# Optimization experiments

Measured on AMD Instinct MI355X. Metric: run time of the kernel, lower is better.

## Reference

```python
import jax, jax.numpy as jnp
import numpy as np

B, S, D = 2, 4096, 768
H, DH = 12, 64
W = 256          # one-sided window (attention_window=512 // 2)
G = 8            # number of global tokens (first G positions)
NEG = -1e9


def setup_inputs() -> dict:
    key = jax.random.key(0)
    ks = jax.random.split(key, 8)
    hidden_states = jax.random.normal(ks[0], (B, S, D), dtype=jnp.float32)
    attention_mask = jnp.ones((B, S), dtype=jnp.float32)
    sc = 0.02
    Wq = jax.random.normal(ks[1], (D, D), dtype=jnp.float32) * sc
    Wk = jax.random.normal(ks[2], (D, D), dtype=jnp.float32) * sc
    Wv = jax.random.normal(ks[3], (D, D), dtype=jnp.float32) * sc
    Wqg = jax.random.normal(ks[4], (D, D), dtype=jnp.float32) * sc
    Wkg = jax.random.normal(ks[5], (D, D), dtype=jnp.float32) * sc
    Wvg = jax.random.normal(ks[6], (D, D), dtype=jnp.float32) * sc
    return {"hidden_states": hidden_states, "attention_mask": attention_mask,
            "Wq": Wq, "Wk": Wk, "Wv": Wv, "Wqg": Wqg, "Wkg": Wkg, "Wvg": Wvg}


def _heads(x):  # [B,S,D] -> [B,H,S,DH]
    return x.reshape(B, S, H, DH).transpose(0, 2, 1, 3)


def longformer_attn(hidden_states, attention_mask, Wq, Wk, Wv, Wqg, Wkg, Wvg):
    scale = 1.0 / jnp.sqrt(jnp.float32(DH))
    q = _heads(hidden_states @ Wq) * scale   # [B,H,S,DH]
    k = _heads(hidden_states @ Wk)
    v = _heads(hidden_states @ Wv)

    n = S // W                                # number of query chunks
    kp = jnp.pad(k, ((0, 0), (0, 0), (W, W), (0, 0)))
    vp = jnp.pad(v, ((0, 0), (0, 0), (W, W), (0, 0)))
    # window indices into padded seq: chunk i covers keys [i*W - W, i*W + 2W)
    idx = jnp.arange(n)[:, None] * W + jnp.arange(3 * W)[None, :]   # [n,3W]
    k_win = kp[:, :, idx]                     # [B,H,n,3W,DH]
    v_win = vp[:, :, idx]
    qc = q.reshape(B, H, n, W, DH)

    scores = jnp.einsum('bhnqd,bhnkd->bhnqk', qc, k_win)  # [B,H,n,W,3W]

    # masks: band (|key-query|<=W), valid key position, not a global key,
    # and key attention_mask
    rel = jnp.arange(3 * W)[None, :] - jnp.arange(W)[:, None]   # [W,3W] = k - q
    band = (rel >= 0) & (rel <= 2 * W)
    key_pos = idx - W                                           # [n,3W] real positions
    valid = (key_pos >= 0) & (key_pos < S) & (key_pos >= G)
    struct_mask = band[None, :, :] & valid[:, None, :]          # [n,W,3W]
    amp = jnp.pad(attention_mask, ((0, 0), (W, W)))
    am_win = amp[:, idx] > 0.5                                  # [B,n,3W]
    full_mask = struct_mask[None] & am_win[:, :, None, :]       # [B,n,W,3W]
    scores = jnp.where(full_mask[:, None], scores, NEG)

    # every query also attends to the G global keys (regular key projection)
    gk = k[:, :, :G]                                            # [B,H,G,DH]
    gscore = jnp.einsum('bhsd,bhgd->bhsg', q, gk).reshape(B, H, n, W, G)
    all_scores = jnp.concatenate([gscore, scores], axis=-1)     # [B,H,n,W,G+3W]
    probs = jax.nn.softmax(all_scores, axis=-1)

    gv = v[:, :, :G]
    out = (jnp.einsum('bhnqk,bhnkd->bhnqd', probs[..., G:], v_win)
           + jnp.einsum('bhnqg,bhgd->bhnqd', probs[..., :G], gv))
    out = out.reshape(B, H, S, DH)

    # global queries attend to ALL tokens with the *_global projections
    qg = _heads(hidden_states @ Wqg)[:, :, :G] * scale          # [B,H,G,DH]
    kg = _heads(hidden_states @ Wkg)
    vg = _heads(hidden_states @ Wvg)
    gs = jnp.einsum('bhgd,bhsd->bhgs', qg, kg)                  # [B,H,G,S]
    gs = jnp.where(attention_mask[:, None, None, :] > 0.5, gs, NEG)
    gp = jax.nn.softmax(gs, axis=-1)
    gout = jnp.einsum('bhgs,bhsd->bhgd', gp, vg)
    out = out.at[:, :, :G].set(gout)

    return out.transpose(0, 2, 1, 3).reshape(B, S, D)


def reference(hidden_states, attention_mask, Wq, Wk, Wv, Wqg, Wkg, Wvg):
    return longformer_attn(hidden_states, attention_mask, Wq, Wk, Wv, Wqg, Wkg, Wvg)
```

## Files before the change

### kernel.cpp

```cpp
#include <hip/hip_runtime.h>

#define B_ 2
#define S_ 4096
#define D_ 768
#define H_ 12
#define DH_ 64
#define W_ 256
#define G_ 8
#define NEG_ (-1e9f)
#define NC_ 64
#define CK_ 64
#define WQB 128
#define NT_ 11
#define NWIN (B_ * H_ * (S_ / WQB))

typedef __attribute__((ext_vector_type(4))) float f32x4;
typedef __attribute__((ext_vector_type(16))) float f32x16;
typedef __attribute__((ext_vector_type(8))) short s16x8;
typedef __attribute__((ext_vector_type(4))) short s16x4;
typedef unsigned short ushort_t;

__device__ __forceinline__ unsigned short f2bf(float f) {
    union { float f; unsigned u; } v; v.f = f;
    unsigned r = v.u + 0x7FFFu + ((v.u >> 16) & 1u);
    return (unsigned short)(r >> 16);
}
__device__ __forceinline__ float bf2f(unsigned short b) {
    union { unsigned u; float f; } v; v.u = ((unsigned)b) << 16;
    return v.f;
}
__device__ __forceinline__ float bfbits(unsigned u) {
    union { unsigned u; float f; } v; v.u = u;
    return v.f;
}
__device__ __forceinline__ unsigned cvtpk_bf16(float lo, float hi) {
    unsigned r;
    asm("v_cvt_pk_bf16_f32 %0, %1, %2" : "=v"(r) : "v"(lo), "v"(hi));
    return r;
}
__device__ __forceinline__ void gload16(const ushort_t* g, ushort_t* l) {
    __builtin_amdgcn_global_load_lds(
        (const __attribute__((address_space(1))) unsigned*)g,
        (__attribute__((address_space(3))) unsigned*)l, 16, 0, 0);
}
__device__ __forceinline__ float vmax16f(f32x16 v) {
    float a0 = fmaxf(v[0], v[1]), a1 = fmaxf(v[2], v[3]);
    float a2 = fmaxf(v[4], v[5]), a3 = fmaxf(v[6], v[7]);
    float a4 = fmaxf(v[8], v[9]), a5 = fmaxf(v[10], v[11]);
    float a6 = fmaxf(v[12], v[13]), a7 = fmaxf(v[14], v[15]);
    return fmaxf(fmaxf(fmaxf(a0, a1), fmaxf(a2, a3)),
                 fmaxf(fmaxf(a4, a5), fmaxf(a6, a7)));
}
__device__ __forceinline__ float vsum16f(f32x16 v) {
    float a0 = v[0] + v[1], a1 = v[2] + v[3];
    float a2 = v[4] + v[5], a3 = v[6] + v[7];
    float a4 = v[8] + v[9], a5 = v[10] + v[11];
    float a6 = v[12] + v[13], a7 = v[14] + v[15];
    return ((a0 + a1) + (a2 + a3)) + ((a4 + a5) + (a6 + a7));
}

__global__ __launch_bounds__(256) void fused_pre(const float* __restrict__ hs,
                                                 const float* __restrict__ W0,
                                                 const float* __restrict__ W1,
                                                 const float* __restrict__ W2,
                                                 const float* __restrict__ W3,
                                                 const float* __restrict__ W4,
                                                 const float* __restrict__ Wqg,
                                                 ushort_t* __restrict__ hs_bf,
                                                 ushort_t* __restrict__ wt,
                                                 float* __restrict__ qg) {
    __shared__ float smf[2 * D_];
    const int bid = blockIdx.x;
    const int t = threadIdx.x;

    if (bid < 3072) {
        const int i = bid * 256 + t;
        float4 a = *(const float4*)&hs[(size_t)i * 8];
        float4 c = *(const float4*)&hs[(size_t)i * 8 + 4];
        s16x8 o;
        o[0] = (short)f2bf(a.x); o[1] = (short)f2bf(a.y);
        o[2] = (short)f2bf(a.z); o[3] = (short)f2bf(a.w);
        o[4] = (short)f2bf(c.x); o[5] = (short)f2bf(c.y);
        o[6] = (short)f2bf(c.z); o[7] = (short)f2bf(c.w);
        *(s16x8*)&hs_bf[(size_t)i * 8] = o;
    } else if (bid < 5952) {
        const int bid2 = bid - 3072;
        const int w = bid2 / 576;
        const int rem = bid2 - w * 576;
        const int k0 = (rem / 24) * 32;
        const int n0 = (rem % 24) * 32;
        const float* Wsrc = (w == 0) ? W0 : (w == 1) ? W1 : (w == 2) ? W2 : (w == 3) ? W3 : W4;
        const float scl = (w == 0) ? 0.125f * 1.44269504f : 1.0f;
        const int r = t >> 3, c4 = (t & 7) * 4;
        float4 src = *(const float4*)&Wsrc[(size_t)(k0 + r) * D_ + n0 + c4];
        smf[r * 33 + c4 + 0] = src.x; smf[r * 33 + c4 + 1] = src.y;
        smf[r * 33 + c4 + 2] = src.z; smf[r * 33 + c4 + 3] = src.w;
        __syncthreads();
        s16x4 o;
        o[0] = (short)f2bf(smf[(c4 + 0) * 33 + r] * scl);
        o[1] = (short)f2bf(smf[(c4 + 1) * 33 + r] * scl);
        o[2] = (short)f2bf(smf[(c4 + 2) * 33 + r] * scl);
        o[3] = (short)f2bf(smf[(c4 + 3) * 33 + r] * scl);
        *(s16x4*)&wt[((size_t)(w * D_ + n0 + r)) * D_ + k0 + c4] = o;
    } else {
        const int bid3 = bid - 5952;
        const int rp = bid3 / 6;
        const int c0 = (bid3 - rp * 6) * 128;
        const int r = t >> 7, cl = t & 127;
        for (int i = t; i < 2 * D_; i += 256) {
            const int rr = i / D_, kk = i - rr * D_;
            const int row = rp * 2 + rr;
            const int b = row >> 3, g = row & 7;
            smf[rr * D_ + kk] = hs[((size_t)b * S_ + g) * D_ + kk];
        }
        __syncthreads();
        float a0 = 0.f, a1 = 0.f, a2 = 0.f, a3 = 0.f;
        const float* wp = &Wqg[c0 + cl];
        for (int kk = 0; kk < D_; kk += 4) {
            a0 += smf[r * D_ + kk + 0] * wp[(size_t)(kk + 0) * D_];
            a1 += smf[r * D_ + kk + 1] * wp[(size_t)(kk + 1) * D_];
            a2 += smf[r * D_ + kk + 2] * wp[(size_t)(kk + 2) * D_];
            a3 += smf[r * D_ + kk + 3] * wp[(size_t)(kk + 3) * D_];
        }
        const int row = rp * 2 + r;
        qg[(size_t)row * D_ + c0 + cl] = (a0 + a1 + a2 + a3) * 0.125f;
    }
}

__global__ __launch_bounds__(256, 2) void proj_mfma(const ushort_t* __restrict__ A,
                                                    const ushort_t* __restrict__ Bt,
                                                    ushort_t* __restrict__ oq,
                                                    ushort_t* __restrict__ ok,
                                                    ushort_t* __restrict__ ov,
                                                    ushort_t* __restrict__ okg,
                                                    ushort_t* __restrict__ ovg) {
    __shared__ char smem[34048];
    ushort_t* Al = (ushort_t*)smem;
    ushort_t* Bl = Al + 128 * 64;

    const int t = threadIdx.x;
    const int m0 = blockIdx.x * 128;
    const int n0 = blockIdx.y * 128;
    const int lane = t & 63;
    const int w = t >> 6;
    const int wm = (w >> 1) * 64, wn = (w & 1) * 64;
    const int ln = lane & 15, hi = lane >> 4;

    const int srow_in_call = lane >> 3;
    const int scol = ((lane & 7) ^ srow_in_call) * 8;

    f32x4 acc[4][4];
#pragma unroll
    for (int mi = 0; mi < 4; ++mi)
#pragma unroll
        for (int ni = 0; ni < 4; ++ni) acc[mi][ni] = (f32x4){0.f, 0.f, 0.f, 0.f};

    for (int k0 = 0; k0 < D_; k0 += 64) {
        __syncthreads();
#pragma unroll
        for (int j = 0; j < 4; ++j) {
            const int rbase = (w * 4 + j) * 8;
            const int row = rbase + srow_in_call;
            gload16(&A[(size_t)(m0 + row) * D_ + k0 + scol], &Al[rbase * 64]);
            gload16(&Bt[(size_t)(n0 + row) * D_ + k0 + scol], &Bl[rbase * 64]);
        }
        __syncthreads();

#pragma unroll
        for (int ks = 0; ks < 2; ++ks) {
            s16x8 af[4], bf[4];
#pragma unroll
            for (int i = 0; i < 4; ++i) {
                const int ar = wm + i * 16 + ln;
                const int br = wn + i * 16 + ln;
                const int slot = (4 * ks + hi) ^ (ln & 7);
                af[i] = *(const s16x8*)&Al[ar * 64 + slot * 8];
                bf[i] = *(const s16x8*)&Bl[br * 64 + slot * 8];
            }
#pragma unroll
            for (int mi = 0; mi < 4; ++mi)
#pragma unroll
                for (int ni = 0; ni < 4; ++ni)
                    acc[mi][ni] = __builtin_amdgcn_mfma_f32_16x16x32_bf16(af[mi], bf[ni], acc[mi][ni], 0, 0, 0);
        }
    }

    float* scr = (float*)smem;
    const int rl = t >> 2, cs = (t & 3) * 32;
    const int ng = n0 + cs;
    const int w_idx = ng / D_;
    const int cb = ng - w_idx * D_;
    const int hh = cb >> 6, dd = cb & 63;
    ushort_t* dst = (w_idx == 0) ? oq : (w_idx == 1) ? ok : (w_idx == 2) ? ov
                    : (w_idx == 3) ? okg : ovg;

#pragma unroll
    for (int r = 0; r < 2; ++r) {
        __syncthreads();
        if ((w >> 1) == r) {
#pragma unroll
            for (int mi = 0; mi < 4; ++mi)
#pragma unroll
                for (int ni = 0; ni < 4; ++ni)
#pragma unroll
                    for (int rr = 0; rr < 4; ++rr)
                        scr[(mi * 16 + hi * 4 + rr) * 132 + wn + ni * 16 + ln] = acc[mi][ni][rr];
        }
        __syncthreads();
        const int m = m0 + r * 64 + rl;
        const int bb = m >> 12, s = m & 4095;
        ushort_t* drow = dst + ((size_t)(bb * H_ + hh) * S_ + s) * DH_ + dd;
        const float* srcp = scr + rl * 132 + cs;
#pragma unroll
        for (int seg = 0; seg < 4; ++seg) {
            float4 lo = *(const float4*)&srcp[seg * 8];
            float4 hi4 = *(const float4*)&srcp[seg * 8 + 4];
            s16x8 o;
            o[0] = (short)f2bf(lo.x); o[1] = (short)f2bf(lo.y);
            o[2] = (short)f2bf(lo.z); o[3] = (short)f2bf(lo.w);
            o[4] = (short)f2bf(hi4.x); o[5] = (short)f2bf(hi4.y);
            o[6] = (short)f2bf(hi4.z); o[7] = (short)f2bf(hi4.w);
            *(s16x8*)&drow[seg * 8] = o;
        }
    }
}

__global__ __launch_bounds__(256, 2) void win_glob(const ushort_t* __restrict__ q,
                                                   const ushort_t* __restrict__ k,
                                                   const ushort_t* __restrict__ v,
                                                   const float* __restrict__ am,
                                                   float* __restrict__ out,
                                                   const float* __restrict__ qg,
                                                   const ushort_t* __restrict__ kg,
                                                   const ushort_t* __restrict__ vg,
                                                   float* __restrict__ pout,
                                                   float* __restrict__ pm,
                                                   float* __restrict__ pl) {
    __shared__ __align__(16) char smem[22016];
    const int bid = blockIdx.x;
    const int t = threadIdx.x;

    if (bid >= NWIN) {
        const int idx = bid - NWIN;
        const int c = idx & 63;
        const int hb = idx >> 6;
        const int h = hb % H_;
        const int b = hb / H_;
        const int bh = b * H_ + h;
        const size_t base = (size_t)bh * S_ * DH_;
        const int jg0 = c * CK_;

        float* qs = (float*)smem;
        ushort_t* kt = (ushort_t*)(smem + 2048);
        ushort_t* vt = (ushort_t*)(smem + 2048 + 9472);
        float* ps = (float*)(smem + 2048 + 9472 + 8448);

        for (int i = t; i < G_ * DH_; i += 256)
            qs[(i >> 6) * DH_ + (i & 63)] = qg[(size_t)(b * G_ + (i >> 6)) * D_ + h * DH_ + (i & 63)];
        {
            const int row = t >> 2, off = (t & 3) * 16;
            const ushort_t* kr = &kg[base + (size_t)(jg0 + row) * DH_ + off];
            const ushort_t* vr = &vg[base + (size_t)(jg0 + row) * DH_ + off];
            union { s16x8 v8; unsigned u[4]; } a0, a1, b0, b1;
            a0.v8 = *(const s16x8*)kr;
            a1.v8 = *(const s16x8*)(kr + 8);
            b0.v8 = *(const s16x8*)vr;
            b1.v8 = *(const s16x8*)(vr + 8);
            unsigned* kd = (unsigned*)&kt[row * 74 + off];
            unsigned* vd = (unsigned*)&vt[row * 66 + off];
#pragma unroll
            for (int i = 0; i < 4; ++i) {
                kd[i] = a0.u[i];
                kd[4 + i] = a1.u[i];
                vd[i] = b0.u[i];
                vd[4 + i] = b1.u[i];
            }
        }
        __syncthreads();

        const int g = t >> 5, jl = t & 31;
        float sc0 = 0.f, sc1 = 0.f;
#pragma unroll 8
        for (int d = 0; d < DH_; d += 2) {
            const unsigned k0p = *(const unsigned*)&kt[jl * 74 + d];
            const unsigned k1p = *(const unsigned*)&kt[(jl + 32) * 74 + d];
            const float q0v = qs[g * DH_ + d];
            const float q1v = qs[g * DH_ + d + 1];
            sc0 += q0v * bfbits(k0p << 16) + q1v * bfbits(k0p & 0xFFFF0000u);
            sc1 += q0v * bfbits(k1p << 16) + q1v * bfbits(k1p & 0xFFFF0000u);
        }
        if (!(am[(size_t)b * S_ + jg0 + jl] > 0.5f)) sc0 = NEG_;
        if (!(am[(size_t)b * S_ + jg0 + jl + 32] > 0.5f)) sc1 = NEG_;

        float mm = fmaxf(sc0, sc1);
        mm = fmaxf(mm, __shfl_xor(mm, 1));
        mm = fmaxf(mm, __shfl_xor(mm, 2));
        mm = fmaxf(mm, __shfl_xor(mm, 4));
        mm = fmaxf(mm, __shfl_xor(mm, 8));
        mm = fmaxf(mm, __shfl_xor(mm, 16));
        const float p0 = __expf(sc0 - mm);
        const float p1 = __expf(sc1 - mm);
        float ls = p0 + p1;
        ls += __shfl_xor(ls, 1);
        ls += __shfl_xor(ls, 2);
        ls += __shfl_xor(ls, 4);
        ls += __shfl_xor(ls, 8);
        ls += __shfl_xor(ls, 16);
        ps[g * CK_ + jl] = p0;
        ps[g * CK_ + jl + 32] = p1;
        if (jl == 0) {
            pm[((size_t)bh * NC_ + c) * G_ + g] = mm;
            pl[((size_t)bh * NC_ + c) * G_ + g] = ls;
        }
        __syncthreads();

#pragma unroll
        for (int pass = 0; pass < 2; ++pass) {
            const int gg = (t >> 6) + pass * 4;
            const int d = t & 63;
            float acc = 0.f;
#pragma unroll 8
            for (int j = 0; j < CK_; ++j) acc += ps[gg * CK_ + j] * bf2f(vt[j * 66 + d]);
            pout[(((size_t)bh * NC_ + c) * G_ + gg) * DH_ + d] = acc;
        }
        return;
    }

    ushort_t* Kl = (ushort_t*)smem;
    ushort_t* Vt = Kl + 64 * 72;
    unsigned* Mv = (unsigned*)(Vt + 64 * 66);
    float* Ow = (float*)smem;

    const int wg = (bid & 7) * 96 + (bid >> 3);
    const int n = wg & 31;
    const int h = (wg >> 5) % H_;
    const int b = wg / (32 * H_);

    const int lane = t & 63, w = t >> 6;
    const int l31 = lane & 31, h5 = lane >> 5;
    const int q0w = n * WQB + w * 32;
    const int q_abs = q0w + l31;
    const size_t bh = (size_t)(b * H_ + h) * S_;

    s16x8 qf[4];
#pragma unroll
    for (int ks = 0; ks < 4; ++ks)
        qf[ks] = *(const s16x8*)&q[(bh + q_abs) * DH_ + ks * 16 + 8 * h5];

    f32x16 oacc[2];
#pragma unroll
    for (int dt = 0; dt < 2; ++dt)
#pragma unroll
        for (int i = 0; i < 16; ++i) oacc[dt][i] = 0.f;
    float m_run, l_run;

    const int srow = t >> 2, soff = (t & 3) * 16;

    {
        const ushort_t* krow = &k[(bh + srow) * DH_ + soff];
        s16x8 k0v = *(const s16x8*)krow;
        s16x8 k1v = *(const s16x8*)(krow + 8);
        *(s16x8*)&Kl[srow * 72 + soff] = k0v;
        *(s16x8*)&Kl[srow * 72 + soff + 8] = k1v;
        const ushort_t* vrow = &v[(bh + srow) * DH_ + soff];
        s16x8 v0v = *(const s16x8*)vrow;
        s16x8 v1v = *(const s16x8*)(vrow + 8);
#pragma unroll
        for (int i = 0; i < 8; ++i) {
            Vt[(soff + i) * 66 + srow] = (ushort_t)v0v[i];
            Vt[(soff + 8 + i) * 66 + srow] = (ushort_t)v1v[i];
        }
    }
    __syncthreads();

    {
        f32x16 s0;
#pragma unroll
        for (int i = 0; i < 16; ++i) s0[i] = 0.f;
#pragma unroll
        for (int ks = 0; ks < 4; ++ks) {
            s16x8 kf = *(const s16x8*)&Kl[l31 * 72 + ks * 16 + 8 * h5];
            s0 = __builtin_amdgcn_mfma_f32_32x32x16_bf16(kf, qf[ks], s0, 0, 0, 0);
        }
        float tmax = fmaxf(fmaxf(s0[0], s0[1]), fmaxf(s0[2], s0[3]));
        tmax = fmaxf(tmax, __shfl_xor(tmax, 32));
        m_run = tmax;
        float p0 = exp2f(s0[0] - m_run), p1 = exp2f(s0[1] - m_run);
        float p2 = exp2f(s0[2] - m_run), p3 = exp2f(s0[3] - m_run);
        float psum = (p0 + p1) + (p2 + p3);
        psum += __shfl_xor(psum, 32);
        l_run = psum;
        const unsigned Au = cvtpk_bf16(p0, p1);
        const unsigned Bu = cvtpk_bf16(p2, p3);
        const unsigned send0 = h5 ? Au : 0u;
        const unsigned send1 = h5 ? Bu : 0u;
        const unsigned recv0 = __shfl_xor((int)send0, 32);
        const unsigned recv1 = __shfl_xor((int)send1, 32);
        union { unsigned u[4]; s16x8 v8; } pu;
        pu.u[0] = h5 ? recv0 : Au;
        pu.u[1] = h5 ? recv1 : Bu;
        pu.u[2] = h5 ? 0u : recv0;
        pu.u[3] = h5 ? 0u : recv1;
#pragma unroll
        for (int dt = 0; dt < 2; ++dt) {
            const int vbase = (dt * 32 + l31) * 66 + 8 * h5;
            union { unsigned u[4]; s16x8 v8; } vf;
            vf.u[0] = *(const unsigned*)&Vt[vbase + 0];
            vf.u[1] = *(const unsigned*)&Vt[vbase + 2];
            vf.u[2] = *(const unsigned*)&Vt[vbase + 4];
            vf.u[3] = *(const unsigned*)&Vt[vbase + 6];
            oacc[dt] = __builtin_amdgcn_mfma_f32_32x32x16_bf16(vf.v8, pu.v8, oacc[dt], 0, 0, 0);
        }
    }

    for (int tt = 1; tt < NT_; ++tt) {
        const int pbase = n * WQB - W_ + (tt - 1) * 64;
        __syncthreads();
        {
            const int p = pbase + srow;
            const int pr = p < 0 ? 0 : (p >= S_ ? S_ - 1 : p);
            const ushort_t* krow = &k[(bh + pr) * DH_ + soff];
            s16x8 k0v = *(const s16x8*)krow;
            s16x8 k1v = *(const s16x8*)(krow + 8);
            *(s16x8*)&Kl[srow * 72 + soff] = k0v;
            *(s16x8*)&Kl[srow * 72 + soff + 8] = k1v;
            const ushort_t* vrow = &v[(bh + pr) * DH_ + soff];
            s16x8 v0v = *(const s16x8*)vrow;
            s16x8 v1v = *(const s16x8*)(vrow + 8);
#pragma unroll
            for (int i = 0; i < 8; ++i) {
                Vt[(soff + i) * 66 + srow] = (ushort_t)v0v[i];
                Vt[(soff + 8 + i) * 66 + srow] = (ushort_t)v1v[i];
            }
        }
        if (w == 0) {
            const int p2 = pbase + lane;
            const bool ok = (p2 >= G_) && (p2 < S_) &&
                            (am[(size_t)b * S_ + (p2 < 0 ? 0 : (p2 >= S_ ? S_ - 1 : p2))] > 0.5f);
            unsigned long long bal = __ballot(ok);
            if (lane == 0) { Mv[0] = (unsigned)bal; Mv[1] = (unsigned)(bal >> 32); }
        }
        __syncthreads();

        if (pbase > q0w + 31 + W_ || pbase + 63 < q0w - W_) continue;

        f32x16 sc[2];
#pragma unroll
        for (int st = 0; st < 2; ++st)
#pragma unroll
            for (int i = 0; i < 16; ++i) sc[st][i] = 0.f;
#pragma unroll
        for (int st = 0; st < 2; ++st)
#pragma unroll
            for (int ks = 0; ks < 4; ++ks) {
                s16x8 kf = *(const s16x8*)&Kl[(st * 32 + l31) * 72 + ks * 16 + 8 * h5];
                sc[st] = __builtin_amdgcn_mfma_f32_32x32x16_bf16(kf, qf[ks], sc[st], 0, 0, 0);
            }

        const unsigned mv0 = Mv[0], mv1 = Mv[1];
        const bool fullt = ((mv0 & mv1) == 0xFFFFFFFFu) &&
                           (pbase >= q0w + 31 - W_) && (pbase + 63 <= q0w + W_);
        if (!fullt) {
#pragma unroll
            for (int st = 0; st < 2; ++st)
#pragma unroll
                for (int reg = 0; reg < 16; ++reg) {
                    const int cst = (reg & 3) + 8 * (reg >> 2);
                    const int crow = cst + 4 * h5;
                    const int key_abs = pbase + st * 32 + crow;
                    const unsigned mvx = (st == 0) ? mv0 : mv1;
                    const bool valid = ((mvx >> crow) & 1u) &&
                                       (key_abs >= q_abs - W_) && (key_abs <= q_abs + W_);
                    sc[st][reg] = valid ? sc[st][reg] : -1e30f;
                }
        }
        float tmax = fmaxf(vmax16f(sc[0]), vmax16f(sc[1]));
        tmax = fmaxf(tmax, __shfl_xor(tmax, 32));

        if (__any(tmax > m_run + 11.5f)) {
            const float mnew = fmaxf(m_run, tmax);
            const float f = exp2f(m_run - mnew);
            l_run *= f;
#pragma unroll
            for (int dt = 0; dt < 2; ++dt)
#pragma unroll
                for (int i = 0; i < 16; ++i) oacc[dt][i] *= f;
            m_run = mnew;
        }
#pragma unroll
        for (int st = 0; st < 2; ++st)
#pragma unroll
            for (int reg = 0; reg < 16; ++reg)
                sc[st][reg] = exp2f(sc[st][reg] - m_run);
        float psum = vsum16f(sc[0]) + vsum16f(sc[1]);
        psum += __shfl_xor(psum, 32);
        l_run += psum;

#pragma unroll
        for (int ks = 0; ks < 4; ++ks) {
            const int st = ks >> 1, k8 = (ks & 1) * 8;
            const unsigned Au = cvtpk_bf16(sc[st][k8 + 0], sc[st][k8 + 1]);
            const unsigned Bu = cvtpk_bf16(sc[st][k8 + 2], sc[st][k8 + 3]);
            const unsigned Cu = cvtpk_bf16(sc[st][k8 + 4], sc[st][k8 + 5]);
            const unsigned Du = cvtpk_bf16(sc[st][k8 + 6], sc[st][k8 + 7]);
            const unsigned send0 = h5 ? Au : Cu;
            const unsigned send1 = h5 ? Bu : Du;
            const unsigned recv0 = __shfl_xor((int)send0, 32);
            const unsigned recv1 = __shfl_xor((int)send1, 32);
            union { unsigned u[4]; s16x8 v8; } pu;
            pu.u[0] = h5 ? recv0 : Au;
            pu.u[1] = h5 ? recv1 : Bu;
            pu.u[2] = h5 ? Cu : recv0;
            pu.u[3] = h5 ? Du : recv1;
#pragma unroll
            for (int dt = 0; dt < 2; ++dt) {
                const int vbase = (dt * 32 + l31) * 66 + ks * 16 + 8 * h5;
                union { unsigned u[4]; s16x8 v8; } vf;
                vf.u[0] = *(const unsigned*)&Vt[vbase + 0];
                vf.u[1] = *(const unsigned*)&Vt[vbase + 2];
                vf.u[2] = *(const unsigned*)&Vt[vbase + 4];
                vf.u[3] = *(const unsigned*)&Vt[vbase + 6];
                oacc[dt] = __builtin_amdgcn_mfma_f32_32x32x16_bf16(vf.v8, pu.v8, oacc[dt], 0, 0, 0);
            }
        }
    }

    const float inv = 1.0f / l_run;
    __syncthreads();
    if (w < 2) {
        float* OwW = Ow + (w & 1) * 32 * 68;
#pragma unroll
        for (int dt = 0; dt < 2; ++dt)
#pragma unroll
            for (int reg = 0; reg < 16; ++reg) {
                const int d = dt * 32 + (reg & 3) + 8 * (reg >> 2) + 4 * h5;
                OwW[l31 * 68 + d] = oacc[dt][reg] * inv;
            }
        asm volatile("s_waitcnt lgkmcnt(0)" ::: "memory");
        const int qq = lane >> 1, half = lane & 1;
        const float* src = &OwW[qq * 68 + half * 32];
        float* dstp = &out[((size_t)b * S_ + q0w + qq) * D_ + h * DH_ + half * 32];
#pragma unroll
        for (int j = 0; j < 8; ++j)
            *(float4*)&dstp[j * 4] = *(const float4*)&src[j * 4];
    }
    __syncthreads();
    if (w >= 2) {
        float* OwW = Ow + (w & 1) * 32 * 68;
#pragma unroll
        for (int dt = 0; dt < 2; ++dt)
#pragma unroll
            for (int reg = 0; reg < 16; ++reg) {
                const int d = dt * 32 + (reg & 3) + 8 * (reg >> 2) + 4 * h5;
                OwW[l31 * 68 + d] = oacc[dt][reg] * inv;
            }
        asm volatile("s_waitcnt lgkmcnt(0)" ::: "memory");
        const int qq = lane >> 1, half = lane & 1;
        const float* src = &OwW[qq * 68 + half * 32];
        float* dstp = &out[((size_t)b * S_ + q0w + qq) * D_ + h * DH_ + half * 32];
#pragma unroll
        for (int j = 0; j < 8; ++j)
            *(float4*)&dstp[j * 4] = *(const float4*)&src[j * 4];
    }
}

__global__ __launch_bounds__(256) void glob_reduce(const float* __restrict__ pout,
                                                   const float* __restrict__ pm,
                                                   const float* __restrict__ pl,
                                                   float* __restrict__ out) {
    const int bh = blockIdx.x;
    const int b = bh / H_, h = bh - b * H_;
    const int t = threadIdx.x;

    __shared__ float wc[G_][NC_];
    __shared__ float wsum[G_];

    const int g = t >> 5, cl = t & 31;
    const float m0 = pm[((size_t)bh * NC_ + cl) * G_ + g];
    const float m1 = pm[((size_t)bh * NC_ + cl + 32) * G_ + g];
    float M = fmaxf(m0, m1);
    M = fmaxf(M, __shfl_xor(M, 1));
    M = fmaxf(M, __shfl_xor(M, 2));
    M = fmaxf(M, __shfl_xor(M, 4));
    M = fmaxf(M, __shfl_xor(M, 8));
    M = fmaxf(M, __shfl_xor(M, 16));
    const float w0 = __expf(m0 - M);
    const float w1 = __expf(m1 - M);
    float S = w0 * pl[((size_t)bh * NC_ + cl) * G_ + g] +
              w1 * pl[((size_t)bh * NC_ + cl + 32) * G_ + g];
    S += __shfl_xor(S, 1);
    S += __shfl_xor(S, 2);
    S += __shfl_xor(S, 4);
    S += __shfl_xor(S, 8);
    S += __shfl_xor(S, 16);
    wc[g][cl] = w0;
    wc[g][cl + 32] = w1;
    if (cl == 0) wsum[g] = S;
    __syncthreads();

#pragma unroll
    for (int pass = 0; pass < 2; ++pass) {
        const int gg = (t >> 6) + pass * 4;
        const int d = t & 63;
        float acc = 0.f;
        for (int c2 = 0; c2 < NC_; ++c2)
            acc += wc[gg][c2] * pout[(((size_t)bh * NC_ + c2) * G_ + gg) * DH_ + d];
        out[((size_t)b * S_ + gg) * D_ + h * DH_ + d] = acc / wsum[gg];
    }
}

extern "C" void kernel_launch(void* const* d_in, const int* in_sizes, int n_in,
                              void* d_out, int out_size, void* d_ws, size_t ws_size,
                              hipStream_t stream) {
    (void)in_sizes; (void)n_in; (void)out_size; (void)ws_size;

    const float* hs    = (const float*)d_in[0];
    const float* amask = (const float*)d_in[1];
    const float* Wq    = (const float*)d_in[2];
    const float* Wk    = (const float*)d_in[3];
    const float* Wv    = (const float*)d_in[4];
    const float* Wqg   = (const float*)d_in[5];
    const float* Wkg   = (const float*)d_in[6];
    const float* Wvg   = (const float*)d_in[7];
    float* out = (float*)d_out;

    char* p = (char*)d_ws;
    ushort_t* hs_bf = (ushort_t*)p; p += (size_t)B_ * S_ * D_ * 2;
    ushort_t* wt    = (ushort_t*)p; p += (size_t)5 * D_ * D_ * 2;
    const size_t per = (size_t)B_ * H_ * S_ * DH_;
    ushort_t* qb  = (ushort_t*)p; p += per * 2;
    ushort_t* kb  = (ushort_t*)p; p += per * 2;
    ushort_t* vb  = (ushort_t*)p; p += per * 2;
    ushort_t* kgb = (ushort_t*)p; p += per * 2;
    ushort_t* vgb = (ushort_t*)p; p += per * 2;
    float* qg   = (float*)p; p += (size_t)B_ * G_ * D_ * 4;
    float* pout = (float*)p; p += (size_t)B_ * H_ * NC_ * G_ * DH_ * 4;
    float* pm   = (float*)p; p += (size_t)B_ * H_ * NC_ * G_ * 4;
    float* pl   = (float*)p;

    fused_pre<<<6000, 256, 0, stream>>>(hs, Wq, Wk, Wv, Wkg, Wvg, Wqg, hs_bf, wt, qg);
    proj_mfma<<<dim3(B_ * S_ / 128, 5 * D_ / 128), 256, 0, stream>>>(hs_bf, wt, qb, kb, vb, kgb, vgb);
    win_glob<<<NWIN + NC_ * H_ * B_, 256, 0, stream>>>(qb, kb, vb, amask, out,
                                                       qg, kgb, vgb, pout, pm, pl);
    glob_reduce<<<B_ * H_, 256, 0, stream>>>(pout, pm, pl, out);
}
```

Before: 140.3 us.

## Overlap global K/V projection with windowed attention in one launch

Splits the projection GEMM so the first launch computes only Q, K and V. The global K and V projection tiles (768 blocks) now share a launch with the windowed attention blocks, so their GEMM work fills the GPU alongside attention. The global-query partial attention moves into its own kernel after that combined launch. This adds a launch, and win_projg's shared memory grows to 34048 bytes for every block, which may lower occupancy of the attention blocks.

```diff
diff --git a/kernel.cpp b/kernel.cpp
--- a/kernel.cpp
+++ b/kernel.cpp
@@ -13,6 +13,7 @@
 #define WQB 128
 #define NT_ 11
 #define NWIN (B_ * H_ * (S_ / WQB))
+#define NPG  768
 
 typedef __attribute__((ext_vector_type(4))) float f32x4;
 typedef __attribute__((ext_vector_type(16))) float f32x16;
@@ -127,20 +128,17 @@
     }
 }
 
-__global__ __launch_bounds__(256, 2) void proj_mfma(const ushort_t* __restrict__ A,
-                                                    const ushort_t* __restrict__ Bt,
-                                                    ushort_t* __restrict__ oq,
-                                                    ushort_t* __restrict__ ok,
-                                                    ushort_t* __restrict__ ov,
-                                                    ushort_t* __restrict__ okg,
-                                                    ushort_t* __restrict__ ovg) {
-    __shared__ char smem[34048];
+__device__ __forceinline__ void proj_body(char* smem, int t, int m0, int n0,
+                                          const ushort_t* __restrict__ A,
+                                          const ushort_t* __restrict__ Bt,
+                                          ushort_t* __restrict__ oq,
+                                          ushort_t* __restrict__ ok,
+                                          ushort_t* __restrict__ ov,
+                                          ushort_t* __restrict__ okg,
+                                          ushort_t* __restrict__ ovg) {
     ushort_t* Al = (ushort_t*)smem;
     ushort_t* Bl = Al + 128 * 64;
 
-    const int t = threadIdx.x;
-    const int m0 = blockIdx.x * 128;
-    const int n0 = blockIdx.y * 128;
     const int lane = t & 63;
     const int w = t >> 6;
     const int wm = (w >> 1) * 64, wn = (w & 1) * 64;
@@ -225,104 +223,34 @@
     }
 }
 
-__global__ __launch_bounds__(256, 2) void win_glob(const ushort_t* __restrict__ q,
-                                                   const ushort_t* __restrict__ k,
-                                                   const ushort_t* __restrict__ v,
-                                                   const float* __restrict__ am,
-                                                   float* __restrict__ out,
-                                                   const float* __restrict__ qg,
-                                                   const ushort_t* __restrict__ kg,
-                                                   const ushort_t* __restrict__ vg,
-                                                   float* __restrict__ pout,
-                                                   float* __restrict__ pm,
-                                                   float* __restrict__ pl) {
-    __shared__ __align__(16) char smem[22016];
+__global__ __launch_bounds__(256, 2) void proj_qkv(const ushort_t* __restrict__ A,
+                                                   const ushort_t* __restrict__ Bt,
+                                                   ushort_t* __restrict__ oq,
+                                                   ushort_t* __restrict__ ok,
+                                                   ushort_t* __restrict__ ov) {
+    __shared__ char smem[34048];
+    proj_body(smem, threadIdx.x, blockIdx.x * 128, blockIdx.y * 128,
+              A, Bt, oq, ok, ov, ov, ov);
+}
+
+__global__ __launch_bounds__(256, 2) void win_projg(const ushort_t* __restrict__ q,
+                                                    const ushort_t* __restrict__ k,
+                                                    const ushort_t* __restrict__ v,
+                                                    const float* __restrict__ am,
+                                                    float* __restrict__ out,
+                                                    const ushort_t* __restrict__ A,
+                                                    const ushort_t* __restrict__ Bt,
+                                                    ushort_t* __restrict__ okg,
+                                                    ushort_t* __restrict__ ovg) {
+    __shared__ __align__(16) char smem[34048];
     const int bid = blockIdx.x;
     const int t = threadIdx.x;
 
     if (bid >= NWIN) {
         const int idx = bid - NWIN;
-        const int c = idx & 63;
-        const int hb = idx >> 6;
-        const int h = hb % H_;
-        const int b = hb / H_;
-        const int bh = b * H_ + h;
-        const size_t base = (size_t)bh * S_ * DH_;
-        const int jg0 = c * CK_;
-
-        float* qs = (float*)smem;
-        ushort_t* kt = (ushort_t*)(smem + 2048);
-        ushort_t* vt = (ushort_t*)(smem + 2048 + 9472);
-        float* ps = (float*)(smem + 2048 + 9472 + 8448);
-
-        for (int i = t; i < G_ * DH_; i += 256)
-            qs[(i >> 6) * DH_ + (i & 63)] = qg[(size_t)(b * G_ + (i >> 6)) * D_ + h * DH_ + (i & 63)];
-        {
-            const int row = t >> 2, off = (t & 3) * 16;
-            const ushort_t* kr = &kg[base + (size_t)(jg0 + row) * DH_ + off];
-            const ushort_t* vr = &vg[base + (size_t)(jg0 + row) * DH_ + off];
-            union { s16x8 v8; unsigned u[4]; } a0, a1, b0, b1;
-            a0.v8 = *(const s16x8*)kr;
-            a1.v8 = *(const s16x8*)(kr + 8);
-            b0.v8 = *(const s16x8*)vr;
-            b1.v8 = *(const s16x8*)(vr + 8);
-            unsigned* kd = (unsigned*)&kt[row * 74 + off];
-            unsigned* vd = (unsigned*)&vt[row * 66 + off];
-#pragma unroll
-            for (int i = 0; i < 4; ++i) {
-                kd[i] = a0.u[i];
-                kd[4 + i] = a1.u[i];
-                vd[i] = b0.u[i];
-                vd[4 + i] = b1.u[i];
-            }
-        }
-        __syncthreads();
-
-        const int g = t >> 5, jl = t & 31;
-        float sc0 = 0.f, sc1 = 0.f;
-#pragma unroll 8
-        for (int d = 0; d < DH_; d += 2) {
-            const unsigned k0p = *(const unsigned*)&kt[jl * 74 + d];
-            const unsigned k1p = *(const unsigned*)&kt[(jl + 32) * 74 + d];
-            const float q0v = qs[g * DH_ + d];
-            const float q1v = qs[g * DH_ + d + 1];
-            sc0 += q0v * bfbits(k0p << 16) + q1v * bfbits(k0p & 0xFFFF0000u);
-            sc1 += q0v * bfbits(k1p << 16) + q1v * bfbits(k1p & 0xFFFF0000u);
-        }
-        if (!(am[(size_t)b * S_ + jg0 + jl] > 0.5f)) sc0 = NEG_;
-        if (!(am[(size_t)b * S_ + jg0 + jl + 32] > 0.5f)) sc1 = NEG_;
-
-        float mm = fmaxf(sc0, sc1);
-        mm = fmaxf(mm, __shfl_xor(mm, 1));
-        mm = fmaxf(mm, __shfl_xor(mm, 2));
-        mm = fmaxf(mm, __shfl_xor(mm, 4));
-        mm = fmaxf(mm, __shfl_xor(mm, 8));
-        mm = fmaxf(mm, __shfl_xor(mm, 16));
-        const float p0 = __expf(sc0 - mm);
-        const float p1 = __expf(sc1 - mm);
-        float ls = p0 + p1;
-        ls += __shfl_xor(ls, 1);
-        ls += __shfl_xor(ls, 2);
-        ls += __shfl_xor(ls, 4);
-        ls += __shfl_xor(ls, 8);
-        ls += __shfl_xor(ls, 16);
-        ps[g * CK_ + jl] = p0;
-        ps[g * CK_ + jl + 32] = p1;
-        if (jl == 0) {
-            pm[((size_t)bh * NC_ + c) * G_ + g] = mm;
-            pl[((size_t)bh * NC_ + c) * G_ + g] = ls;
-        }
-        __syncthreads();
-
-#pragma unroll
-        for (int pass = 0; pass < 2; ++pass) {
-            const int gg = (t >> 6) + pass * 4;
-            const int d = t & 63;
-            float acc = 0.f;
-#pragma unroll 8
-            for (int j = 0; j < CK_; ++j) acc += ps[gg * CK_ + j] * bf2f(vt[j * 66 + d]);
-            pout[(((size_t)bh * NC_ + c) * G_ + gg) * DH_ + d] = acc;
-        }
+        const int m0 = (idx / 12) * 128;
+        const int n0 = 3 * D_ + (idx % 12) * 128;
+        proj_body(smem, t, m0, n0, A, Bt, okg, okg, okg, okg, ovg);
         return;
     }
 
@@ -561,6 +489,95 @@
 #pragma unroll
         for (int j = 0; j < 8; ++j)
             *(float4*)&dstp[j * 4] = *(const float4*)&src[j * 4];
+    }
+}
+
+__global__ __launch_bounds__(256) void glob_partial(const float* __restrict__ qg,
+                                                    const ushort_t* __restrict__ kg,
+                                                    const ushort_t* __restrict__ vg,
+                                                    const float* __restrict__ am,
+                                                    float* __restrict__ pout,
+                                                    float* __restrict__ pm,
+                                                    float* __restrict__ pl) {
+    const int c = blockIdx.x, h = blockIdx.y, b = blockIdx.z;
+    const int t = threadIdx.x;
+    const int bh = b * H_ + h;
+    const size_t base = (size_t)bh * S_ * DH_;
+    const int jg0 = c * CK_;
+
+    __shared__ __align__(16) char smem[22016];
+    float* qs = (float*)smem;
+    ushort_t* kt = (ushort_t*)(smem + 2048);
+    ushort_t* vt = (ushort_t*)(smem + 2048 + 9472);
+    float* ps = (float*)(smem + 2048 + 9472 + 8448);
+
+    for (int i = t; i < G_ * DH_; i += 256)
+        qs[(i >> 6) * DH_ + (i & 63)] = qg[(size_t)(b * G_ + (i >> 6)) * D_ + h * DH_ + (i & 63)];
+    {
+        const int row = t >> 2, off = (t & 3) * 16;
+        const ushort_t* kr = &kg[base + (size_t)(jg0 + row) * DH_ + off];
+        const ushort_t* vr = &vg[base + (size_t)(jg0 + row) * DH_ + off];
+        union { s16x8 v8; unsigned u[4]; } a0, a1, b0, b1;
+        a0.v8 = *(const s16x8*)kr;
+        a1.v8 = *(const s16x8*)(kr + 8);
+        b0.v8 = *(const s16x8*)vr;
+        b1.v8 = *(const s16x8*)(vr + 8);
+        unsigned* kd = (unsigned*)&kt[row * 74 + off];
+        unsigned* vd = (unsigned*)&vt[row * 66 + off];
+#pragma unroll
+        for (int i = 0; i < 4; ++i) {
+            kd[i] = a0.u[i];
+            kd[4 + i] = a1.u[i];
+            vd[i] = b0.u[i];
+            vd[4 + i] = b1.u[i];
+        }
+    }
+    __syncthreads();
+
+    const int g = t >> 5, jl = t & 31;
+    float sc0 = 0.f, sc1 = 0.f;
+#pragma unroll 8
+    for (int d = 0; d < DH_; d += 2) {
+        const unsigned k0p = *(const unsigned*)&kt[jl * 74 + d];
+        const unsigned k1p = *(const unsigned*)&kt[(jl + 32) * 74 + d];
+        const float q0v = qs[g * DH_ + d];
+        const float q1v = qs[g * DH_ + d + 1];
+        sc0 += q0v * bfbits(k0p << 16) + q1v * bfbits(k0p & 0xFFFF0000u);
+        sc1 += q0v * bfbits(k1p << 16) + q1v * bfbits(k1p & 0xFFFF0000u);
+    }
+    if (!(am[(size_t)b * S_ + jg0 + jl] > 0.5f)) sc0 = NEG_;
+    if (!(am[(size_t)b * S_ + jg0 + jl + 32] > 0.5f)) sc1 = NEG_;
+
+    float mm = fmaxf(sc0, sc1);
+    mm = fmaxf(mm, __shfl_xor(mm, 1));
+    mm = fmaxf(mm, __shfl_xor(mm, 2));
+    mm = fmaxf(mm, __shfl_xor(mm, 4));
+    mm = fmaxf(mm, __shfl_xor(mm, 8));
+    mm = fmaxf(mm, __shfl_xor(mm, 16));
+    const float p0 = __expf(sc0 - mm);
+    const float p1 = __expf(sc1 - mm);
+    float ls = p0 + p1;
+    ls += __shfl_xor(ls, 1);
+    ls += __shfl_xor(ls, 2);
+    ls += __shfl_xor(ls, 4);
+    ls += __shfl_xor(ls, 8);
+    ls += __shfl_xor(ls, 16);
+    ps[g * CK_ + jl] = p0;
+    ps[g * CK_ + jl + 32] = p1;
+    if (jl == 0) {
+        pm[((size_t)bh * NC_ + c) * G_ + g] = mm;
+        pl[((size_t)bh * NC_ + c) * G_ + g] = ls;
+    }
+    __syncthreads();
+
+#pragma unroll
+    for (int pass = 0; pass < 2; ++pass) {
+        const int gg = (t >> 6) + pass * 4;
+        const int d = t & 63;
+        float acc = 0.f;
+#pragma unroll 8
+        for (int j = 0; j < CK_; ++j) acc += ps[gg * CK_ + j] * bf2f(vt[j * 66 + d]);
+        pout[(((size_t)bh * NC_ + c) * G_ + gg) * DH_ + d] = acc;
     }
 }
 
@@ -639,8 +656,8 @@
     float* pl   = (float*)p;
 
     fused_pre<<<6000, 256, 0, stream>>>(hs, Wq, Wk, Wv, Wkg, Wvg, Wqg, hs_bf, wt, qg);
-    proj_mfma<<<dim3(B_ * S_ / 128, 5 * D_ / 128), 256, 0, stream>>>(hs_bf, wt, qb, kb, vb, kgb, vgb);
-    win_glob<<<NWIN + NC_ * H_ * B_, 256, 0, stream>>>(qb, kb, vb, amask, out,
-                                                       qg, kgb, vgb, pout, pm, pl);
+    proj_qkv<<<dim3(B_ * S_ / 128, 3 * D_ / 128), 256, 0, stream>>>(hs_bf, wt, qb, kb, vb);
+    win_projg<<<NWIN + NPG, 256, 0, stream>>>(qb, kb, vb, amask, out, hs_bf, wt, kgb, vgb);
+    glob_partial<<<dim3(NC_, H_, B_), 256, 0, stream>>>(qg, kgb, vgb, amask, pout, pm, pl);
     glob_reduce<<<B_ * H_, 256, 0, stream>>>(pout, pm, pl, out);
 }
```

Result: slower. 152.5 us (+8.7%).
